# Optimization experiments

Measured on AMD Instinct MI355X. Metric: run time of the kernel, lower is better.

## Reference

```python
import jax, jax.numpy as jnp
import numpy as np

B, C, H, W = 8, 128, 64, 64
C8, C2 = C // 8, C // 2


def conv1x1(x, w, b):
    # x: [B,Cin,H,W], w: [Cout,Cin], b: [Cout]
    return jnp.einsum('bchw,oc->bohw', x, w) + b[None, :, None, None]


def maxpool2(x):
    # 2x2 stride-2 max pool on [B,C,H,W]
    b, c, h, w = x.shape
    return x.reshape(b, c, h // 2, 2, w // 2, 2).max(axis=(3, 5))


def setup_inputs() -> dict:
    key = jax.random.key(0)
    ks = jax.random.split(key, 10)
    s_in = 1.0 / np.sqrt(C)
    s_c2 = 1.0 / np.sqrt(C2)
    return {
        'x': jax.random.normal(ks[0], (B, C, H, W), dtype=jnp.float32),
        'w_theta': jax.random.uniform(ks[1], (C8, C), jnp.float32, -s_in, s_in),
        'b_theta': jax.random.uniform(ks[2], (C8,), jnp.float32, -s_in, s_in),
        'w_phi': jax.random.uniform(ks[3], (C8, C), jnp.float32, -s_in, s_in),
        'b_phi': jax.random.uniform(ks[4], (C8,), jnp.float32, -s_in, s_in),
        'w_g': jax.random.uniform(ks[5], (C2, C), jnp.float32, -s_in, s_in),
        'b_g': jax.random.uniform(ks[6], (C2,), jnp.float32, -s_in, s_in),
        'w_attn': jax.random.uniform(ks[7], (C, C2), jnp.float32, -s_c2, s_c2),
        'b_attn': jax.random.uniform(ks[8], (C,), jnp.float32, -s_c2, s_c2),
        'sigma': jnp.zeros((1,), dtype=jnp.float32),
    }


def reference(x, w_theta, b_theta, w_phi, b_phi, w_g, b_g, w_attn, b_attn, sigma):
    b, ch, h, w = x.shape
    n, m = h * w, (h * w) // 4
    theta = conv1x1(x, w_theta, b_theta).reshape(b, ch // 8, n)          # [B,C8,N]
    phi = maxpool2(conv1x1(x, w_phi, b_phi)).reshape(b, ch // 8, m)      # [B,C8,M]
    attn = jax.nn.softmax(jnp.einsum('bdn,bdm->bnm', theta, phi), axis=-1)  # [B,N,M]
    g = maxpool2(conv1x1(x, w_g, b_g)).reshape(b, ch // 2, m)            # [B,C2,M]
    attn_g = jnp.einsum('bcm,bnm->bcn', g, attn).reshape(b, ch // 2, h, w)
    attn_g = conv1x1(attn_g, w_attn, b_attn)
    return x + sigma[0] * attn_g
```

## Files before the change

### kernel.cpp

```cpp
#include <hip/hip_runtime.h>
#include <hip/hip_bf16.h>
#include <math.h>
#include <string.h>

#define Bn 8
#define Cn 128
#define Nn 4096
#define Mn 1024
#define C8n 16
#define C2n 64

typedef __attribute__((ext_vector_type(8))) short short8;
typedef __attribute__((ext_vector_type(4))) float floatx4;
typedef __attribute__((ext_vector_type(4))) unsigned short ushortx4;

typedef const __attribute__((address_space(1))) void gv_t;
typedef __attribute__((address_space(3))) void lv_t;

__device__ __forceinline__ unsigned short f2bf(float f) {
    union { float f; unsigned u; } v; v.f = f;
    unsigned r = v.u + 0x7fff + ((v.u >> 16) & 1);
    return (unsigned short)(r >> 16);
}
__device__ __forceinline__ unsigned pk2(float a, float b) {
    __hip_bfloat162 h = __float22bfloat162_rn(make_float2(a, b));
    union { __hip_bfloat162 h2; unsigned u; } cv;
    cv.h2 = h;
    return cv.u;
}

__global__ __launch_bounds__(256) void k1_pre(
    const float* __restrict__ x,
    const float* __restrict__ w_theta, const float* __restrict__ b_theta,
    const float* __restrict__ w_phi,   const float* __restrict__ b_phi,
    const float* __restrict__ w_g,     const float* __restrict__ b_g,
    unsigned short* __restrict__ thA,
    unsigned short* __restrict__ phB,
    unsigned short* __restrict__ gB)
{
    __shared__ unsigned short wA[6 * 4 * 64 * 8];
    __shared__ unsigned short xB[8 * 4 * 64 * 8];
    __shared__ unsigned short pool[80][33];
    __shared__ float biases[96];

    const int t    = threadIdx.x;
    const int b    = blockIdx.x & 7;
    const int h2   = blockIdx.x >> 3;
    const int wv   = t >> 6;
    const int lane = t & 63;
    const int q    = lane >> 4;
    const int l15  = lane & 15;
    const float L2E = 1.4426950408889634f;

    if (t < 96)
        biases[t] = (t < 16) ? b_theta[t] * L2E
                  : (t < 32) ? b_phi[t - 16] : b_g[t - 32];

    #pragma unroll
    for (int k = 0; k < 12; ++k) {
        int u  = t + k * 256;
        int oc = u >> 5, c4 = u & 31;
        const float* src = (oc < 16) ? (w_theta + oc * Cn)
                         : (oc < 32) ? (w_phi + (oc - 16) * Cn)
                                     : (w_g + (oc - 32) * Cn);
        float4 wv4 = *(const float4*)(src + c4 * 4);
        float sc = (oc < 16) ? L2E : 1.f;
        int c = c4 * 4;
        int ot = oc >> 4, kc = c >> 5, qq = (c >> 3) & 3, jj = c & 7;
        uint2 pk = { pk2(wv4.x * sc, wv4.y * sc), pk2(wv4.z * sc, wv4.w * sc) };
        *(uint2*)(wA + (((ot * 4 + kc) * 64 + qq * 16 + (oc & 15)) * 8 + jj)) = pk;
    }

    const float* xb = x + (size_t)b * Cn * Nn + h2 * 128;
    #pragma unroll
    for (int k = 0; k < 16; ++k) {
        int u   = t + k * 256;
        int pos = u & 127, c4 = u >> 7;
        int c   = c4 * 4;
        float v0 = xb[(size_t)(c + 0) * Nn + pos];
        float v1 = xb[(size_t)(c + 1) * Nn + pos];
        float v2 = xb[(size_t)(c + 2) * Nn + pos];
        float v3 = xb[(size_t)(c + 3) * Nn + pos];
        int pt = pos >> 4, kc = c >> 5, qq = (c >> 3) & 3, jj = c & 7;
        uint2 pk = { pk2(v0, v1), pk2(v2, v3) };
        *(uint2*)(xB + (((pt * 4 + kc) * 64 + qq * 16 + (pos & 15)) * 8 + jj)) = pk;
    }
    __syncthreads();

    floatx4 acc[6][2];
    #pragma unroll
    for (int ot = 0; ot < 6; ++ot)
        #pragma unroll
        for (int p2 = 0; p2 < 2; ++p2) acc[ot][p2] = (floatx4){0.f, 0.f, 0.f, 0.f};

    #pragma unroll
    for (int kc = 0; kc < 4; ++kc) {
        short8 Bf0 = *(const short8*)(xB + ((wv * 4 + kc) * 64 + lane) * 8);
        short8 Bf1 = *(const short8*)(xB + (((wv + 4) * 4 + kc) * 64 + lane) * 8);
        #pragma unroll
        for (int ot = 0; ot < 6; ++ot) {
            short8 Af = *(const short8*)(wA + ((ot * 4 + kc) * 64 + lane) * 8);
            acc[ot][0] = __builtin_amdgcn_mfma_f32_16x16x32_bf16(Af, Bf0, acc[ot][0], 0, 0, 0);
            acc[ot][1] = __builtin_amdgcn_mfma_f32_16x16x32_bf16(Af, Bf1, acc[ot][1], 0, 0, 0);
        }
    }

    #pragma unroll
    for (int p2 = 0; p2 < 2; ++p2) {
        const int pt = wv + p2 * 4;
        float v0 = acc[0][p2][0] + biases[q * 4 + 0];
        float v1 = acc[0][p2][1] + biases[q * 4 + 1];
        float v2 = acc[0][p2][2] + biases[q * 4 + 2];
        float v3 = acc[0][p2][3] + biases[q * 4 + 3];
        uint2 pk = { pk2(v0, v1), pk2(v2, v3) };
        *(uint2*)(thA + ((((size_t)b * 256 + h2 * 8 + pt) * 2 + (q >> 1)) * 128
                         + l15 * 8 + (q & 1) * 4)) = pk;
    }

    #pragma unroll
    for (int ot = 1; ot < 6; ++ot) {
        #pragma unroll
        for (int r = 0; r < 4; ++r) {
            float vmax = fmaxf(acc[ot][0][r], acc[ot][1][r]);
            float pmax = fmaxf(vmax, __shfl_xor(vmax, 1, 64));
            if ((l15 & 1) == 0) {
                int oc = (ot - 1) * 16 + q * 4 + r;
                int w2 = wv * 8 + (l15 >> 1);
                pool[oc][w2] = f2bf(pmax + biases[16 + oc]);
            }
        }
    }
    __syncthreads();

    if (t < 64) {
        int w2h = t >> 5, ml = (t >> 1) & 15, dh = t & 1;
        int w2 = w2h * 16 + ml;
        ushortx4 lo, hi;
        #pragma unroll
        for (int j = 0; j < 4; ++j) { lo[j] = pool[dh * 8 + j][w2];
                                      hi[j] = pool[dh * 8 + 4 + j][w2]; }
        unsigned short* dst = phB + (((size_t)b * 64 + h2 * 2 + w2h) * 2 + dh) * 128 + ml * 8;
        *(ushortx4*)dst = lo;
        *(ushortx4*)(dst + 4) = hi;
    }
    {
        int c = t >> 2, sq = t & 3;
        ushortx4 lo, hi;
        #pragma unroll
        for (int j = 0; j < 8; ++j) {
            int w2 = (j & 1) * 16 + sq * 4 + (j >> 1);
            unsigned short v = pool[16 + c][w2];
            if (j < 4) lo[j] = v; else hi[j - 4] = v;
        }
        unsigned short* dst = gB + ((((size_t)b * 32 + h2) * 4 + (c >> 4)) * 4 + sq) * 128
                              + (c & 15) * 8;
        *(ushortx4*)dst = lo;
        *(ushortx4*)(dst + 4) = hi;
    }
}

__global__ __launch_bounds__(256, 2) void k2_attn(
    const float* __restrict__ x,
    const unsigned short* __restrict__ thA,
    const unsigned short* __restrict__ phB,
    const unsigned short* __restrict__ gB,
    const float* __restrict__ w_attn, const float* __restrict__ b_attn,
    const float* __restrict__ sigma_p,
    float* __restrict__ out)
{
    __shared__ __attribute__((aligned(16))) char smem[58880];
    char* buf0  = smem;
    char* buf1  = smem + 20480;
    char* Pall  = smem + 40960;
    float* battn = (float*)(smem + 58368);

    const int tid  = threadIdx.x;
    const int wave = tid >> 6;
    const int lane = tid & 63;
    const int q    = lane >> 4;
    const int l15  = lane & 15;
    const int b    = blockIdx.x & 7;
    const int n0   = (blockIdx.x >> 3) * 64;
    const int nw   = n0 + wave * 16;
    char* Pbase = Pall + wave * 4352;

    const float sg = sigma_p[0];

    short8 thf = {};
    if (q < 2)
        thf = *(const short8*)(thA + ((((size_t)b * 256 + (nw >> 4)) * 2 + q) * 16 + l15) * 8);

    floatx4 O[4];
    #pragma unroll
    for (int cs = 0; cs < 4; ++cs) O[cs] = (floatx4){0.f, 0.f, 0.f, 0.f};
    float L[4] = {0.f, 0.f, 0.f, 0.f};

    const char* phb = (const char*)(phB + (size_t)b * 16384);
    const char* gbb = (const char*)(gB  + (size_t)b * 65536);

    for (int j = wave; j < 20; j += 4) {
        const char* src = (j < 4) ? (phb + j * 1024) : (gbb + (j - 4) * 1024);
        __builtin_amdgcn_global_load_lds((gv_t*)(src + lane * 16),
                                         (lv_t*)(buf0 + j * 1024), 16, 0, 0);
    }

    for (int s = 0; s < 8; ++s) {
        __syncthreads();
        if (s < 7) {
            char* nbuf = (s & 1) ? buf0 : buf1;
            const char* php = phb + (size_t)(s + 1) * 4096;
            const char* gp  = gbb + (size_t)(s + 1) * 16384;
            for (int j = wave; j < 20; j += 4) {
                const char* src = (j < 4) ? (php + j * 1024) : (gp + (j - 4) * 1024);
                __builtin_amdgcn_global_load_lds((gv_t*)(src + lane * 16),
                                                 (lv_t*)(nbuf + j * 1024), 16, 0, 0);
            }
        }
        const char* cbuf = (s & 1) ? buf1 : buf0;
        const unsigned short* phis = (const unsigned short*)cbuf;
        const unsigned short* gs   = (const unsigned short*)(cbuf + 4096);

        #pragma unroll
        for (int g2 = 0; g2 < 4; ++g2) {
            short8 bf0 = {}, bf1 = {};
            if (q < 2) {
                bf0 = *(const short8*)(phis + (((2 * g2)     * 2 + q) * 16 + l15) * 8);
                bf1 = *(const short8*)(phis + (((2 * g2 + 1) * 2 + q) * 16 + l15) * 8);
            }
            floatx4 S0 = __builtin_amdgcn_mfma_f32_16x16x32_bf16(
                             thf, bf0, (floatx4){0.f, 0.f, 0.f, 0.f}, 0, 0, 0);
            floatx4 S1 = __builtin_amdgcn_mfma_f32_16x16x32_bf16(
                             thf, bf1, (floatx4){0.f, 0.f, 0.f, 0.f}, 0, 0, 0);
            #pragma unroll
            for (int r = 0; r < 4; ++r) {
                float pa = exp2f(S0[r]);
                float pb = exp2f(S1[r]);
                L[r] += pa + pb;
                *(unsigned*)(Pbase + (q * 4 + r) * 272 + g2 * 64 + l15 * 4) = pk2(pa, pb);
            }
        }

        #pragma unroll
        for (int ch = 0; ch < 4; ++ch) {
            short8 Af = *(const short8*)(Pbase + l15 * 272 + ch * 64 + q * 16);
            const unsigned short* gchunk = gs + ch * 2048;
            #pragma unroll
            for (int cs = 0; cs < 4; ++cs) {
                short8 Bf = *(const short8*)(gchunk + ((cs * 4 + q) * 16 + l15) * 8);
                O[cs] = __builtin_amdgcn_mfma_f32_16x16x32_bf16(Af, Bf, O[cs], 0, 0, 0);
            }
        }
    }

    #pragma unroll
    for (int d = 1; d <= 8; d <<= 1)
        #pragma unroll
        for (int r = 0; r < 4; ++r) L[r] += __shfl_xor(L[r], d, 64);

    __syncthreads();
    {
        unsigned short* wAe = (unsigned short*)smem;
        #pragma unroll
        for (int k = 0; k < 8; ++k) {
            int i = tid + k * 256;
            float4 wv = ((const float4*)w_attn)[i];
            int o = i >> 4, c = (i & 15) * 4;
            uint2 pk = { pk2(wv.x, wv.y), pk2(wv.z, wv.w) };
            *(uint2*)(wAe + ((o >> 4) * 2 + (c >> 5)) * 512 + (o & 15) * 32 + (c & 31)) = pk;
        }
        if (tid < 128) battn[tid] = b_attn[tid];
    }
    {
        float inv[4];
        #pragma unroll
        for (int r = 0; r < 4; ++r) inv[r] = 1.0f / L[r];
        unsigned short* Ob = (unsigned short*)Pbase;
        #pragma unroll
        for (int cs = 0; cs < 4; ++cs)
            #pragma unroll
            for (int r = 0; r < 4; ++r)
                Ob[(q * 4 + r) * 72 + cs * 16 + l15] = f2bf(O[cs][r] * inv[r]);
    }
    __syncthreads();

    {
        unsigned short* wAe = (unsigned short*)smem;
        unsigned short* Ob = (unsigned short*)Pbase;
        short8 B0 = *(const short8*)(Ob + l15 * 72 + q * 8);
        short8 B1 = *(const short8*)(Ob + l15 * 72 + 32 + q * 8);
        const float* xw = x   + (size_t)b * Cn * Nn + nw + l15;
        float*       ow = out + (size_t)b * Cn * Nn + nw + l15;
        #pragma unroll
        for (int ot = 0; ot < 8; ++ot) {
            short8 A0 = *(const short8*)(wAe + (ot * 2 + 0) * 512 + l15 * 32 + q * 8);
            short8 A1 = *(const short8*)(wAe + (ot * 2 + 1) * 512 + l15 * 32 + q * 8);
            floatx4 D = __builtin_amdgcn_mfma_f32_16x16x32_bf16(
                            A0, B0, (floatx4){0.f, 0.f, 0.f, 0.f}, 0, 0, 0);
            D = __builtin_amdgcn_mfma_f32_16x16x32_bf16(A1, B1, D, 0, 0, 0);
            #pragma unroll
            for (int r = 0; r < 4; ++r) {
                int o = ot * 16 + q * 4 + r;
                float v = D[r] + battn[o];
                ow[(size_t)o * Nn] = xw[(size_t)o * Nn] + sg * v;
            }
        }
    }
}

extern "C" void kernel_launch(void* const* d_in, const int* in_sizes, int n_in,
                              void* d_out, int out_size, void* d_ws, size_t ws_size,
                              hipStream_t stream) {
    const float* x       = (const float*)d_in[0];
    const float* w_theta = (const float*)d_in[1];
    const float* b_theta = (const float*)d_in[2];
    const float* w_phi   = (const float*)d_in[3];
    const float* b_phi   = (const float*)d_in[4];
    const float* w_g     = (const float*)d_in[5];
    const float* b_g     = (const float*)d_in[6];
    const float* w_attn  = (const float*)d_in[7];
    const float* b_attn  = (const float*)d_in[8];
    const float* sigma   = (const float*)d_in[9];
    float* out = (float*)d_out;

    unsigned short* thA = (unsigned short*)d_ws;
    unsigned short* phB = thA + 524288;
    unsigned short* gBp = phB + 131072;

    k1_pre<<<256, 256, 0, stream>>>(x, w_theta, b_theta, w_phi, b_phi,
                                    w_g, b_g, thA, phB, gBp);
    k2_attn<<<512, 256, 0, stream>>>(x, thA, phB, gBp, w_attn, b_attn, sigma, out);
}
```

Baseline: 115.2 us.

## Split key range across wave pairs in attention kernel to double block count

Each block now handles 32 query rows instead of 64. The four waves form two pairs, and each pair processes half of the M keys in 16 smaller stages. The partial O and L results are reduced through shared memory, and the output projection is split across the halves. Shared memory per block shrinks and launch bounds rise to four blocks per CU, with twice as many blocks launched. The aim is more occupancy and parallelism to hide latency, at the cost of an extra reduction, extra barriers, and double the phi/g loads per query row.

```diff
diff --git a/kernel.cpp b/kernel.cpp
--- a/kernel.cpp
+++ b/kernel.cpp
@@ -159,7 +159,7 @@
     }
 }
 
-__global__ __launch_bounds__(256, 2) void k2_attn(
+__global__ __launch_bounds__(256, 4) void k2_attn(
     const float* __restrict__ x,
     const unsigned short* __restrict__ thA,
     const unsigned short* __restrict__ phB,
@@ -168,11 +168,9 @@
     const float* __restrict__ sigma_p,
     float* __restrict__ out)
 {
-    __shared__ __attribute__((aligned(16))) char smem[58880];
-    char* buf0  = smem;
-    char* buf1  = smem + 20480;
-    char* Pall  = smem + 40960;
-    float* battn = (float*)(smem + 58368);
+    __shared__ __attribute__((aligned(16))) char smem[26112];
+    char*  Pall  = smem + 20480;
+    float* battn = (float*)(smem + 25600);
 
     const int tid  = threadIdx.x;
     const int wave = tid >> 6;
@@ -180,15 +178,18 @@
     const int q    = lane >> 4;
     const int l15  = lane & 15;
     const int b    = blockIdx.x & 7;
-    const int n0   = (blockIdx.x >> 3) * 64;
-    const int nw   = n0 + wave * 16;
-    char* Pbase = Pall + wave * 4352;
+    const int nb   = blockIdx.x >> 3;
+    const int t    = wave & 1;
+    const int h    = wave >> 1;
+    const int ntile = nb * 2 + t;
+    const int nw   = ntile * 16;
+    char* Pbase = Pall + wave * 1280;
 
     const float sg = sigma_p[0];
 
     short8 thf = {};
     if (q < 2)
-        thf = *(const short8*)(thA + ((((size_t)b * 256 + (nw >> 4)) * 2 + q) * 16 + l15) * 8);
+        thf = *(const short8*)(thA + ((((size_t)b * 256 + ntile) * 2 + q) * 16 + l15) * 8);
 
     floatx4 O[4];
     #pragma unroll
@@ -197,67 +198,101 @@
 
     const char* phb = (const char*)(phB + (size_t)b * 16384);
     const char* gbb = (const char*)(gB  + (size_t)b * 65536);
-
-    for (int j = wave; j < 20; j += 4) {
-        const char* src = (j < 4) ? (phb + j * 1024) : (gbb + (j - 4) * 1024);
-        __builtin_amdgcn_global_load_lds((gv_t*)(src + lane * 16),
-                                         (lv_t*)(buf0 + j * 1024), 16, 0, 0);
-    }
-
-    for (int s = 0; s < 8; ++s) {
+    const char* sph = phb + h * 16384;
+    const char* sgb = gbb + h * 65536;
+    char* mybuf = smem + h * 10240;
+
+    {
+        const char* srcp = sph;
+        const char* srcg = sgb;
+        char* dst = mybuf;
+        for (int j = t; j < 5; j += 2) {
+            const char* src = (j == 0) ? srcp : (srcg + (j - 1) * 1024);
+            __builtin_amdgcn_global_load_lds((gv_t*)(src + lane * 16),
+                                             (lv_t*)(dst + j * 1024), 16, 0, 0);
+        }
+    }
+
+    for (int s = 0; s < 16; ++s) {
         __syncthreads();
-        if (s < 7) {
-            char* nbuf = (s & 1) ? buf0 : buf1;
-            const char* php = phb + (size_t)(s + 1) * 4096;
-            const char* gp  = gbb + (size_t)(s + 1) * 16384;
-            for (int j = wave; j < 20; j += 4) {
-                const char* src = (j < 4) ? (php + j * 1024) : (gp + (j - 4) * 1024);
+        if (s < 15) {
+            char* dst = mybuf + ((s + 1) & 1) * 5120;
+            const char* srcp = sph + (s + 1) * 1024;
+            const char* srcg = sgb + (size_t)(s + 1) * 4096;
+            for (int j = t; j < 5; j += 2) {
+                const char* src = (j == 0) ? srcp : (srcg + (j - 1) * 1024);
                 __builtin_amdgcn_global_load_lds((gv_t*)(src + lane * 16),
-                                                 (lv_t*)(nbuf + j * 1024), 16, 0, 0);
+                                                 (lv_t*)(dst + j * 1024), 16, 0, 0);
             }
         }
-        const char* cbuf = (s & 1) ? buf1 : buf0;
+        const char* cbuf = mybuf + (s & 1) * 5120;
         const unsigned short* phis = (const unsigned short*)cbuf;
-        const unsigned short* gs   = (const unsigned short*)(cbuf + 4096);
-
-        #pragma unroll
-        for (int g2 = 0; g2 < 4; ++g2) {
-            short8 bf0 = {}, bf1 = {};
-            if (q < 2) {
-                bf0 = *(const short8*)(phis + (((2 * g2)     * 2 + q) * 16 + l15) * 8);
-                bf1 = *(const short8*)(phis + (((2 * g2 + 1) * 2 + q) * 16 + l15) * 8);
-            }
-            floatx4 S0 = __builtin_amdgcn_mfma_f32_16x16x32_bf16(
-                             thf, bf0, (floatx4){0.f, 0.f, 0.f, 0.f}, 0, 0, 0);
-            floatx4 S1 = __builtin_amdgcn_mfma_f32_16x16x32_bf16(
-                             thf, bf1, (floatx4){0.f, 0.f, 0.f, 0.f}, 0, 0, 0);
+        const unsigned short* gs   = (const unsigned short*)(cbuf + 1024);
+
+        short8 bf0 = {}, bf1 = {};
+        if (q < 2) {
+            bf0 = *(const short8*)(phis + ((0 * 2 + q) * 16 + l15) * 8);
+            bf1 = *(const short8*)(phis + ((1 * 2 + q) * 16 + l15) * 8);
+        }
+        floatx4 S0 = __builtin_amdgcn_mfma_f32_16x16x32_bf16(
+                         thf, bf0, (floatx4){0.f, 0.f, 0.f, 0.f}, 0, 0, 0);
+        floatx4 S1 = __builtin_amdgcn_mfma_f32_16x16x32_bf16(
+                         thf, bf1, (floatx4){0.f, 0.f, 0.f, 0.f}, 0, 0, 0);
+        #pragma unroll
+        for (int r = 0; r < 4; ++r) {
+            float pa = exp2f(S0[r]);
+            float pb = exp2f(S1[r]);
+            L[r] += pa + pb;
+            *(unsigned*)(Pbase + (q * 4 + r) * 80 + l15 * 4) = pk2(pa, pb);
+        }
+
+        short8 Af = *(const short8*)(Pbase + l15 * 80 + q * 16);
+        #pragma unroll
+        for (int cs = 0; cs < 4; ++cs) {
+            short8 Bf = *(const short8*)(gs + ((cs * 4 + q) * 16 + l15) * 8);
+            O[cs] = __builtin_amdgcn_mfma_f32_16x16x32_bf16(Af, Bf, O[cs], 0, 0, 0);
+        }
+    }
+
+    #pragma unroll
+    for (int d = 1; d <= 8; d <<= 1)
+        #pragma unroll
+        for (int r = 0; r < 4; ++r) L[r] += __shfl_xor(L[r], d, 64);
+
+    __syncthreads();
+    float* Lpart = (float*)(smem + 8704);
+    if (h == 1) {
+        #pragma unroll
+        for (int r = 0; r < 4; ++r) {
+            float* Orow = (float*)(smem + t * 4352 + (q * 4 + r) * 272);
             #pragma unroll
-            for (int r = 0; r < 4; ++r) {
-                float pa = exp2f(S0[r]);
-                float pb = exp2f(S1[r]);
-                L[r] += pa + pb;
-                *(unsigned*)(Pbase + (q * 4 + r) * 272 + g2 * 64 + l15 * 4) = pk2(pa, pb);
-            }
-        }
-
-        #pragma unroll
-        for (int ch = 0; ch < 4; ++ch) {
-            short8 Af = *(const short8*)(Pbase + l15 * 272 + ch * 64 + q * 16);
-            const unsigned short* gchunk = gs + ch * 2048;
+            for (int cs = 0; cs < 4; ++cs) Orow[cs * 16 + l15] = O[cs][r];
+            if (l15 == 0) Lpart[t * 16 + q * 4 + r] = L[r];
+        }
+    }
+    if (tid < 128) battn[tid] = b_attn[tid];
+    __syncthreads();
+    unsigned short* Obuf = (unsigned short*)(smem + 20480);
+    if (h == 0) {
+        #pragma unroll
+        for (int r = 0; r < 4; ++r) {
+            const float* Orow = (const float*)(smem + t * 4352 + (q * 4 + r) * 272);
             #pragma unroll
-            for (int cs = 0; cs < 4; ++cs) {
-                short8 Bf = *(const short8*)(gchunk + ((cs * 4 + q) * 16 + l15) * 8);
-                O[cs] = __builtin_amdgcn_mfma_f32_16x16x32_bf16(Af, Bf, O[cs], 0, 0, 0);
-            }
-        }
-    }
-
-    #pragma unroll
-    for (int d = 1; d <= 8; d <<= 1)
-        #pragma unroll
-        for (int r = 0; r < 4; ++r) L[r] += __shfl_xor(L[r], d, 64);
-
-    __syncthreads();
+            for (int cs = 0; cs < 4; ++cs) O[cs][r] += Orow[cs * 16 + l15];
+            L[r] += Lpart[t * 16 + q * 4 + r];
+        }
+        float inv[4];
+        #pragma unroll
+        for (int r = 0; r < 4; ++r) inv[r] = 1.0f / L[r];
+        unsigned short* Ob = Obuf + t * 1152;
+        #pragma unroll
+        for (int cs = 0; cs < 4; ++cs)
+            #pragma unroll
+            for (int r = 0; r < 4; ++r)
+                Ob[(q * 4 + r) * 72 + cs * 16 + l15] = f2bf(O[cs][r] * inv[r]);
+    }
+    __syncthreads();
+
     {
         unsigned short* wAe = (unsigned short*)smem;
         #pragma unroll
@@ -268,30 +303,19 @@
             uint2 pk = { pk2(wv.x, wv.y), pk2(wv.z, wv.w) };
             *(uint2*)(wAe + ((o >> 4) * 2 + (c >> 5)) * 512 + (o & 15) * 32 + (c & 31)) = pk;
         }
-        if (tid < 128) battn[tid] = b_attn[tid];
-    }
+    }
+    __syncthreads();
+
     {
-        float inv[4];
-        #pragma unroll
-        for (int r = 0; r < 4; ++r) inv[r] = 1.0f / L[r];
-        unsigned short* Ob = (unsigned short*)Pbase;
-        #pragma unroll
-        for (int cs = 0; cs < 4; ++cs)
-            #pragma unroll
-            for (int r = 0; r < 4; ++r)
-                Ob[(q * 4 + r) * 72 + cs * 16 + l15] = f2bf(O[cs][r] * inv[r]);
-    }
-    __syncthreads();
-
-    {
-        unsigned short* wAe = (unsigned short*)smem;
-        unsigned short* Ob = (unsigned short*)Pbase;
+        const unsigned short* wAe = (const unsigned short*)smem;
+        const unsigned short* Ob  = Obuf + t * 1152;
         short8 B0 = *(const short8*)(Ob + l15 * 72 + q * 8);
         short8 B1 = *(const short8*)(Ob + l15 * 72 + 32 + q * 8);
         const float* xw = x   + (size_t)b * Cn * Nn + nw + l15;
         float*       ow = out + (size_t)b * Cn * Nn + nw + l15;
         #pragma unroll
-        for (int ot = 0; ot < 8; ++ot) {
+        for (int ot4 = 0; ot4 < 4; ++ot4) {
+            const int ot = h * 4 + ot4;
             short8 A0 = *(const short8*)(wAe + (ot * 2 + 0) * 512 + l15 * 32 + q * 8);
             short8 A1 = *(const short8*)(wAe + (ot * 2 + 1) * 512 + l15 * 32 + q * 8);
             floatx4 D = __builtin_amdgcn_mfma_f32_16x16x32_bf16(
@@ -328,5 +352,5 @@
 
     k1_pre<<<256, 256, 0, stream>>>(x, w_theta, b_theta, w_phi, b_phi,
                                     w_g, b_g, thA, phB, gBp);
-    k2_attn<<<512, 256, 0, stream>>>(x, thA, phB, gBp, w_attn, b_attn, sigma, out);
-}
+    k2_attn<<<1024, 256, 0, stream>>>(x, thA, phB, gBp, w_attn, b_attn, sigma, out);
+}
```

After: 115.7 us. Within noise of the previous version (+0.4%).
